# Optimization experiments

Hardware: AMD Instinct MI355X
Metric: run time of the kernel (lower is better)

The kernel has to match this reference:

```python
import jax, jax.numpy as jnp
import numpy as np

DIM = 256
HEADS = 8
HEAD_DIM = DIM // HEADS
WS = 8
EPS = 1e-5


def layernorm(x, g, b):
    mu = jnp.mean(x, axis=-1, keepdims=True)
    var = jnp.var(x, axis=-1, keepdims=True)
    return (x - mu) * jax.lax.rsqrt(var + EPS) * g + b


def partition_windows(x, ws):
    B, H, W, C = x.shape
    x = x.reshape(B, H // ws, ws, W // ws, ws, C)
    x = jnp.transpose(x, (0, 1, 3, 2, 4, 5))
    return x.reshape(B * (H // ws) * (W // ws), ws * ws, C)


def unpartition_windows(x, ws, B, H, W):
    C = x.shape[-1]
    x = x.reshape(B, H // ws, W // ws, ws, ws, C)
    x = jnp.transpose(x, (0, 1, 3, 2, 4, 5))
    return x.reshape(B, H, W, C)


def setup_inputs() -> dict:
    key = jax.random.key(0)
    ks = jax.random.split(key, 14)
    B, H, W, C = 16, 64, 64, DIM
    s_in = 1.0 / np.sqrt(C)
    s_hid = 1.0 / np.sqrt(4 * C)
    return {
        "x": jax.random.normal(ks[0], (B, H, W, C), jnp.float32),
        "ln1_g": jnp.ones((C,), jnp.float32),
        "ln1_b": jnp.zeros((C,), jnp.float32),
        "qkv_w": jax.random.uniform(ks[1], (3 * C, C), jnp.float32, -s_in, s_in),
        "qkv_b": jax.random.uniform(ks[2], (3 * C,), jnp.float32, -s_in, s_in),
        "proj_w": jax.random.uniform(ks[3], (C, C), jnp.float32, -s_in, s_in),
        "proj_b": jax.random.uniform(ks[4], (C,), jnp.float32, -s_in, s_in),
        "ln2_g": jnp.ones((C,), jnp.float32),
        "ln2_b": jnp.zeros((C,), jnp.float32),
        "ffn_w1": jax.random.uniform(ks[5], (4 * C, C), jnp.float32, -s_in, s_in),
        "ffn_b1": jax.random.uniform(ks[6], (4 * C,), jnp.float32, -s_in, s_in),
        "ffn_w2": jax.random.uniform(ks[7], (C, 4 * C), jnp.float32, -s_hid, s_hid),
        "ffn_b2": jax.random.uniform(ks[8], (C,), jnp.float32, -s_hid, s_hid),
    }


def attention(blocks, qkv_w, qkv_b, proj_w, proj_b):
    # blocks: [Bn, N, C]
    Bn, N, C = blocks.shape
    qkv = blocks @ qkv_w.T + qkv_b  # [Bn, N, 3C]
    qkv = qkv.reshape(Bn, N, 3, HEADS, HEAD_DIM)
    q, k, v = qkv[:, :, 0], qkv[:, :, 1], qkv[:, :, 2]  # each [Bn, N, h, d]
    # Faithful to the source: q @ k^T over the last two dims -> head-x-head scores per token
    scores = jnp.einsum("bnhd,bngd->bnhg", q, k) / np.sqrt(HEAD_DIM)
    attn = jax.nn.softmax(scores, axis=-1)
    out = jnp.einsum("bnhg,bngd->bnhd", attn, v).reshape(Bn, N, C)
    return out @ proj_w.T + proj_b


def reference(x, ln1_g, ln1_b, qkv_w, qkv_b, proj_w, proj_b,
              ln2_g, ln2_b, ffn_w1, ffn_b1, ffn_w2, ffn_b2):
    B, H, W, C = x.shape
    x_ = layernorm(x, ln1_g, ln1_b)
    blocks = partition_windows(x_, WS)  # [B*nW, ws*ws, C]
    out = attention(blocks, qkv_w, qkv_b, proj_w, proj_b)
    x = x + unpartition_windows(out, WS, B, H, W)
    x_ = layernorm(x, ln2_g, ln2_b)
    x_ = jax.nn.relu(x_ @ ffn_w1.T + ffn_b1) @ ffn_w2.T + ffn_b2
    return x + x_
```

## Files before the change

### kernel.cpp

```cpp
#include <hip/hip_runtime.h>
#include <hip/hip_bf16.h>
#include <stdint.h>

typedef float f32x4 __attribute__((ext_vector_type(4)));
typedef __bf16 bf16x8 __attribute__((ext_vector_type(8)));
typedef unsigned short ushort8 __attribute__((ext_vector_type(8)));

__device__ __forceinline__ float bf2f(unsigned short u) {
    unsigned int x = ((unsigned int)u) << 16;
    return __builtin_bit_cast(float, x);
}
__device__ __forceinline__ unsigned short f2bf(float f) {
    unsigned int x = __builtin_bit_cast(unsigned int, f);
    unsigned int lsb = (x >> 16) & 1u;
    x += 0x7fffu + lsb;
    return (unsigned short)(x >> 16);
}

#define GLL16(gptr, lptr)                                                      \
    __builtin_amdgcn_global_load_lds(                                          \
        (const __attribute__((address_space(1))) void*)(gptr),                 \
        (__attribute__((address_space(3))) void*)(lptr), 16, 0, 0)

__global__ __launch_bounds__(256) void cvt4_kernel(
    const float* __restrict__ w0, const float* __restrict__ w1,
    const float* __restrict__ w2, const float* __restrict__ w3,
    unsigned short* __restrict__ dst)
{
    const int i = blockIdx.x * 256 + threadIdx.x;
    const float* s; int off;
    if      (i <  49152) { s = w0; off = 0; }
    else if (i <  65536) { s = w1; off = 49152; }
    else if (i < 131072) { s = w2; off = 65536; }
    else                 { s = w3; off = 131072; }
    f32x4 v = ((const f32x4*)s)[i - off];
    ushort4 o;
    o.x = f2bf(v.x); o.y = f2bf(v.y); o.z = f2bf(v.z); o.w = f2bf(v.w);
    ((ushort4*)dst)[i] = o;
}

__global__ __launch_bounds__(256) void ln_kernel(
    const float* __restrict__ x, const float* __restrict__ g,
    const float* __restrict__ b, unsigned short* __restrict__ y)
{
    const int lane = threadIdx.x & 63, wave = threadIdx.x >> 6;
    const size_t tok = (size_t)blockIdx.x * 4 + wave;
    f32x4 v = *(const f32x4*)(x + tok * 256 + lane * 4);
    float s = v.x + v.y + v.z + v.w;
    float q = v.x * v.x + v.y * v.y + v.z * v.z + v.w * v.w;
#pragma unroll
    for (int o = 32; o; o >>= 1) {
        s += __shfl_xor(s, o, 64);
        q += __shfl_xor(q, o, 64);
    }
    float mean = s * (1.f / 256.f);
    float var  = q * (1.f / 256.f) - mean * mean;
    float rstd = rsqrtf(var + 1e-5f);
    f32x4 gr = *(const f32x4*)(g + lane * 4);
    f32x4 br = *(const f32x4*)(b + lane * 4);
    ushort4 o4;
    o4.x = f2bf((v.x - mean) * rstd * gr.x + br.x);
    o4.y = f2bf((v.y - mean) * rstd * gr.y + br.y);
    o4.z = f2bf((v.z - mean) * rstd * gr.z + br.z);
    o4.w = f2bf((v.w - mean) * rstd * gr.w + br.w);
    *(ushort4*)(y + tok * 256 + lane * 4) = o4;
}

template <int RELU, int HASRES, int OUTF32>
__global__ __launch_bounds__(256) void gemm_bt(
    const unsigned short* __restrict__ A,
    const unsigned short* __restrict__ W,
    const float* __restrict__ bias,
    const float* res,
    void* Cv,
    int M, int N, int K, int nby)
{
    __shared__ __align__(16) unsigned short As[128 * 64];
    __shared__ __align__(16) unsigned short Bs[128 * 64];

    const int t    = threadIdx.x;
    const int id   = blockIdx.x;
    const int xcd  = id & 7;
    const int sl   = id >> 3;
    const int by   = sl % nby;
    const int bx   = (sl / nby) * 8 + xcd;
    const int m0   = bx * 128;
    const int n0   = by * 128;
    const int lane = t & 63;
    const int wave = t >> 6;
    const int wm = wave & 1, wn = wave >> 1;
    const int lr = lane & 15, kc = lane >> 4;

    f32x4 acc[4][4] = {};

    const int rA   = t >> 3;
    const int gcol = ((t & 7) ^ (rA & 7)) * 8;
    const unsigned short* gA = A + (size_t)(m0 + rA) * K + gcol;
    const unsigned short* gB = W + (size_t)(n0 + rA) * K + gcol;

    for (int k0 = 0; k0 < K; k0 += 64) {
#pragma unroll
        for (int w = 0; w < 4; ++w) {
            GLL16(gA + (size_t)(w * 32) * K + k0, &As[(w * 256 + t) * 8]);
            GLL16(gB + (size_t)(w * 32) * K + k0, &Bs[(w * 256 + t) * 8]);
        }
        __syncthreads();

#pragma unroll
        for (int hh = 0; hh < 2; ++hh) {
            bf16x8 af[4], bf[4];
#pragma unroll
            for (int i = 0; i < 4; ++i) {
                const int ra = wm * 64 + i * 16 + lr;
                const int rb = wn * 64 + i * 16 + lr;
                af[i] = *(const bf16x8*)&As[ra * 64 + ((hh * 4 + kc) ^ (ra & 7)) * 8];
                bf[i] = *(const bf16x8*)&Bs[rb * 64 + ((hh * 4 + kc) ^ (rb & 7)) * 8];
            }
#pragma unroll
            for (int i = 0; i < 4; ++i)
#pragma unroll
                for (int j = 0; j < 4; ++j)
                    acc[i][j] = __builtin_amdgcn_mfma_f32_16x16x32_bf16(
                        af[i], bf[j], acc[i][j], 0, 0, 0);
        }
        __syncthreads();
    }

    float* Cf = (float*)Cv;
    unsigned short* Cb = (unsigned short*)Cv;
    const int row0 = m0 + wm * 64;
    const int col0 = n0 + wn * 64;
    const int cl = lane & 15;
    const int rq = (lane >> 4) * 4;
#pragma unroll
    for (int i = 0; i < 4; ++i) {
#pragma unroll
        for (int j = 0; j < 4; ++j) {
            const int col = col0 + j * 16 + cl;
            const float bv = bias[col];
#pragma unroll
            for (int r = 0; r < 4; ++r) {
                const int row = row0 + i * 16 + rq + r;
                float v = acc[i][j][r] + bv;
                if (RELU) v = fmaxf(v, 0.f);
                const size_t o = (size_t)row * N + col;
                if (HASRES) v += res[o];
                if (OUTF32) Cf[o] = v;
                else        Cb[o] = f2bf(v);
            }
        }
    }
}

__global__ __launch_bounds__(256) void attn_headmix(
    const unsigned short* __restrict__ qkv,
    unsigned short* __restrict__ out,
    int T)
{
    const int lane = threadIdx.x & 63, wave = threadIdx.x >> 6;
    const int tok = blockIdx.x * 4 + wave;
    if (tok >= T) return;
    const unsigned short* base = qkv + (size_t)tok * 768;
    const int h = lane >> 3, g = lane & 7;

    float s = 0.f;
#pragma unroll
    for (int d8 = 0; d8 < 4; ++d8) {
        ushort4 qa = *(const ushort4*)(base + h * 32 + d8 * 8);
        ushort4 qb = *(const ushort4*)(base + h * 32 + d8 * 8 + 4);
        ushort4 ka = *(const ushort4*)(base + 256 + g * 32 + d8 * 8);
        ushort4 kb = *(const ushort4*)(base + 256 + g * 32 + d8 * 8 + 4);
        s += bf2f(qa.x) * bf2f(ka.x) + bf2f(qa.y) * bf2f(ka.y)
           + bf2f(qa.z) * bf2f(ka.z) + bf2f(qa.w) * bf2f(ka.w)
           + bf2f(qb.x) * bf2f(kb.x) + bf2f(qb.y) * bf2f(kb.y)
           + bf2f(qb.z) * bf2f(kb.z) + bf2f(qb.w) * bf2f(kb.w);
    }
    s *= 0.17677669529663687f;

    float mx = s;
#pragma unroll
    for (int o = 1; o < 8; o <<= 1) mx = fmaxf(mx, __shfl_xor(mx, o, 64));
    float e = __expf(s - mx);
    float sum = e;
#pragma unroll
    for (int o = 1; o < 8; o <<= 1) sum += __shfl_xor(sum, o, 64);
    const float a = e / sum;

    float o0 = 0.f, o1 = 0.f, o2 = 0.f, o3 = 0.f;
#pragma unroll
    for (int gg = 0; gg < 8; ++gg) {
        const float ag = __shfl(a, (lane & 56) | gg, 64);
        ushort4 vv = *(const ushort4*)(base + 512 + gg * 32 + g * 4);
        o0 += ag * bf2f(vv.x);
        o1 += ag * bf2f(vv.y);
        o2 += ag * bf2f(vv.z);
        o3 += ag * bf2f(vv.w);
    }
    ushort4 ov;
    ov.x = f2bf(o0); ov.y = f2bf(o1); ov.z = f2bf(o2); ov.w = f2bf(o3);
    *(ushort4*)(out + (size_t)tok * 256 + lane * 4) = ov;
}

__global__ __launch_bounds__(512, 2) void ffn_fused(
    float* xo,
    const float* __restrict__ ln2_g, const float* __restrict__ ln2_b,
    const unsigned short* __restrict__ w1,
    const float* __restrict__ b1p,
    const unsigned short* __restrict__ w2,
    const float* __restrict__ b2p)
{
    __shared__ __align__(16) unsigned short U[32768];
    __shared__ __align__(16) unsigned short W1a[16384];
    __shared__ __align__(16) unsigned short W2a[16384];
    __shared__ __align__(16) unsigned short Hs[2][8192];

    unsigned short* const W1b = U;
    unsigned short* const W2b = U + 16384;

    const int t = threadIdx.x;
    const int lane = t & 63, wave = t >> 6;
    const int m0 = blockIdx.x * 128;
    const int lr = lane & 15, kc = lane >> 4;
    const int cl = lane & 15, rq = (lane >> 4) * 4;
    const int wm = wave & 1, wn = wave >> 1;

    const int r1b = t >> 5;
    const int sc1 = t & 31;
    const int gc1 = (sc1 & ~7) | ((sc1 & 7) ^ (r1b & 7));
    const int r2b = t >> 3;
    const int gc2 = (t & 7) ^ (r2b & 7);

    #define STAGE_W1(hp, W1t)                                                  \
        do {                                                                   \
            _Pragma("unroll")                                                  \
            for (int j = 0; j < 4; ++j)                                        \
                GLL16(w1 + (size_t)((hp) * 64 + j * 16 + r1b) * 256 + gc1 * 8, \
                      &(W1t)[(j * 512 + t) * 8]);                              \
        } while (0)
    #define STAGE_W2(hp, W2t)                                                  \
        do {                                                                   \
            _Pragma("unroll")                                                  \
            for (int j = 0; j < 4; ++j)                                        \
                GLL16(w2 + (size_t)(j * 64 + r2b) * 1024 + (hp) * 64 + gc2 * 8,\
                      &(W2t)[(j * 512 + t) * 8]);                              \
        } while (0)

    STAGE_W1(0, W1a);
    STAGE_W2(0, W2a);

    {
        const int row0 = t >> 2;
        const int seg  = t & 3;
        const float* xrp = xo + (size_t)(m0 + row0) * 256 + seg * 64;
        f32x4 xv[16];
#pragma unroll
        for (int i = 0; i < 16; ++i) xv[i] = ((const f32x4*)xrp)[i];
        float s = 0.f, q = 0.f;
#pragma unroll
        for (int i = 0; i < 16; ++i) {
            s += xv[i].x + xv[i].y + xv[i].z + xv[i].w;
            q += xv[i].x * xv[i].x + xv[i].y * xv[i].y
               + xv[i].z * xv[i].z + xv[i].w * xv[i].w;
        }
        s += __shfl_xor(s, 1, 64); q += __shfl_xor(q, 1, 64);
        s += __shfl_xor(s, 2, 64); q += __shfl_xor(q, 2, 64);
        const float mean = s * (1.f / 256.f);
        const float rstd = rsqrtf(q * (1.f / 256.f) - mean * mean + 1e-5f);
#pragma unroll
        for (int c8 = 0; c8 < 8; ++c8) {
            const f32x4 g0 = ((const f32x4*)(ln2_g + seg * 64 + c8 * 8))[0];
            const f32x4 g1 = ((const f32x4*)(ln2_g + seg * 64 + c8 * 8))[1];
            const f32x4 bb0 = ((const f32x4*)(ln2_b + seg * 64 + c8 * 8))[0];
            const f32x4 bb1 = ((const f32x4*)(ln2_b + seg * 64 + c8 * 8))[1];
            const f32x4 a0 = xv[c8 * 2], a1 = xv[c8 * 2 + 1];
            ushort8 o;
            o[0] = f2bf((a0.x - mean) * rstd * g0.x + bb0.x);
            o[1] = f2bf((a0.y - mean) * rstd * g0.y + bb0.y);
            o[2] = f2bf((a0.z - mean) * rstd * g0.z + bb0.z);
            o[3] = f2bf((a0.w - mean) * rstd * g0.w + bb0.w);
            o[4] = f2bf((a1.x - mean) * rstd * g1.x + bb1.x);
            o[5] = f2bf((a1.y - mean) * rstd * g1.y + bb1.y);
            o[6] = f2bf((a1.z - mean) * rstd * g1.z + bb1.z);
            o[7] = f2bf((a1.w - mean) * rstd * g1.w + bb1.w);
            const int gc = seg * 8 + c8;
            const int sc = (gc & ~7) | ((gc & 7) ^ (row0 & 7));
            *(ushort8*)&U[row0 * 256 + sc * 8] = o;
        }
    }
    __syncthreads();

    bf16x8 afr[4][8];
#pragma unroll
    for (int i = 0; i < 4; ++i) {
        const int ra = wm * 64 + i * 16 + lr;
#pragma unroll
        for (int ks = 0; ks < 8; ++ks) {
            const int c = ks * 4 + kc;
            afr[i][ks] = *(const bf16x8*)
                &U[ra * 256 + ((c & ~7) | ((c & 7) ^ (ra & 7))) * 8];
        }
    }
    __syncthreads();
    STAGE_W1(1, W1b);

    f32x4 acc[4][4] = {};

    #define HPHASE(hcv, W1c, Hbuf)                                             \
        do {                                                                   \
            f32x4 acch[4] = {};                                                \
            __builtin_amdgcn_s_setprio(1);                                     \
            _Pragma("unroll")                                                  \
            for (int ks = 0; ks < 8; ++ks) {                                   \
                const int c = ks * 4 + kc;                                     \
                const int rb = wn * 16 + lr;                                   \
                const bf16x8 bfr = *(const bf16x8*)                            \
                    &(W1c)[rb * 256 + ((c & ~7) | ((c & 7) ^ (rb & 7))) * 8];  \
                _Pragma("unroll")                                              \
                for (int i = 0; i < 4; ++i)                                    \
                    acch[i] = __builtin_amdgcn_mfma_f32_16x16x32_bf16(         \
                        bfr, afr[i][ks], acch[i], 0, 0, 0);                    \
            }                                                                  \
            __builtin_amdgcn_s_setprio(0);                                     \
            const f32x4 bv = *(const f32x4*)(b1p + (hcv) * 64 + wn * 16 + rq); \
            const int sbase = wn * 2 + (rq >> 3);                              \
            _Pragma("unroll")                                                  \
            for (int i = 0; i < 4; ++i) {                                      \
                const int tok = wm * 64 + i * 16 + cl;                         \
                ushort4 o;                                                     \
                o.x = f2bf(fmaxf(acch[i][0] + bv.x, 0.f));                     \
                o.y = f2bf(fmaxf(acch[i][1] + bv.y, 0.f));                     \
                o.z = f2bf(fmaxf(acch[i][2] + bv.z, 0.f));                     \
                o.w = f2bf(fmaxf(acch[i][3] + bv.w, 0.f));                     \
                *(ushort4*)&(Hbuf)[tok * 64 + ((sbase ^ (tok & 7)) * 8)        \
                                   + (rq & 4)] = o;                            \
            }                                                                  \
        } while (0)

    #define OPHASE(W2c, Hbuf)                                                  \
        do {                                                                   \
            _Pragma("unroll")                                                  \
            for (int ks = 0; ks < 2; ++ks) {                                   \
                const int c = ks * 4 + kc;                                     \
                bf16x8 bw[4];                                                  \
                _Pragma("unroll")                                              \
                for (int j = 0; j < 4; ++j) {                                  \
                    const int rb = wn * 64 + j * 16 + lr;                      \
                    bw[j] = *(const bf16x8*)                                   \
                        &(W2c)[rb * 64 + ((c ^ (rb & 7)) * 8)];                \
                }                                                              \
                __builtin_amdgcn_s_setprio(1);                                 \
                _Pragma("unroll")                                              \
                for (int i = 0; i < 4; ++i) {                                  \
                    const int ra = wm * 64 + i * 16 + lr;                      \
                    const bf16x8 ah = *(const bf16x8*)                         \
                        &(Hbuf)[ra * 64 + ((c ^ (ra & 7)) * 8)];               \
                    _Pragma("unroll")                                          \
                    for (int j = 0; j < 4; ++j)                                \
                        acc[i][j] = __builtin_amdgcn_mfma_f32_16x16x32_bf16(   \
                            ah, bw[j], acc[i][j], 0, 0, 0);                    \
                }                                                              \
                __builtin_amdgcn_s_setprio(0);                                 \
            }                                                                  \
        } while (0)

    HPHASE(0, W1a, Hs[0]);
    __syncthreads();

    for (int hc = 0; hc < 16; ++hc) {
        if (hc < 14) STAGE_W1(hc + 2, (hc & 1) ? W1b : W1a);
        if (hc < 15) STAGE_W2(hc + 1, (hc & 1) ? W2a : W2b);
        if (hc < 15) HPHASE(hc + 1, (hc & 1) ? W1a : W1b, Hs[(hc + 1) & 1]);
        OPHASE((hc & 1) ? W2b : W2a, Hs[hc & 1]);
        __syncthreads();
    }

    const int rqe = (lane >> 4) * 4;
#pragma unroll
    for (int i = 0; i < 4; ++i)
#pragma unroll
        for (int j = 0; j < 4; ++j) {
            const int col = wn * 64 + j * 16 + cl;
            const float bv = b2p[col];
#pragma unroll
            for (int r = 0; r < 4; ++r) {
                const int row = m0 + wm * 64 + i * 16 + rqe + r;
                const size_t o = (size_t)row * 256 + col;
                xo[o] = acc[i][j][r] + bv + xo[o];
            }
        }
    #undef STAGE_W1
    #undef STAGE_W2
    #undef HPHASE
    #undef OPHASE
}

extern "C" void kernel_launch(void* const* d_in, const int* in_sizes, int n_in,
                              void* d_out, int out_size, void* d_ws, size_t ws_size,
                              hipStream_t stream)
{
    const float* x      = (const float*)d_in[0];
    const float* ln1_g  = (const float*)d_in[1];
    const float* ln1_b  = (const float*)d_in[2];
    const float* qkv_w  = (const float*)d_in[3];
    const float* qkv_b  = (const float*)d_in[4];
    const float* proj_w = (const float*)d_in[5];
    const float* proj_b = (const float*)d_in[6];
    const float* ln2_g  = (const float*)d_in[7];
    const float* ln2_b  = (const float*)d_in[8];
    const float* ffn_w1 = (const float*)d_in[9];
    const float* ffn_b1 = (const float*)d_in[10];
    const float* ffn_w2 = (const float*)d_in[11];
    const float* ffn_b2 = (const float*)d_in[12];
    float* xo = (float*)d_out;

    const int M = 65536;
    const size_t MEG = 1024 * 1024;
    unsigned short* ws = (unsigned short*)d_ws;
    unsigned short* qkv_wb  = ws;
    unsigned short* proj_wb = ws + 196608;
    unsigned short* ffn_w1b = ws + 262144;
    unsigned short* ffn_w2b = ws + 524288;
    unsigned short* xn   = ws + 1 * MEG;
    unsigned short* att  = ws + 17 * MEG;
    unsigned short* qkvb = ws + 33 * MEG;

    cvt4_kernel<<<768, 256, 0, stream>>>(qkv_w, proj_w, ffn_w1, ffn_w2, ws);

    ln_kernel<<<M / 4, 256, 0, stream>>>(x, ln1_g, ln1_b, xn);
    gemm_bt<0, 0, 0><<<3072, 256, 0, stream>>>(
        xn, qkv_wb, qkv_b, nullptr, qkvb, M, 768, 256, 6);
    attn_headmix<<<M / 4, 256, 0, stream>>>(qkvb, att, M);
    gemm_bt<0, 1, 1><<<1024, 256, 0, stream>>>(
        att, proj_wb, proj_b, x, xo, M, 256, 256, 2);
    ffn_fused<<<M / 128, 512, 0, stream>>>(
        xo, ln2_g, ln2_b, ffn_w1b, ffn_b1, ffn_w2b, ffn_b2);
}
```

Baseline: 413.7 us.

## Use partial vmcnt waits and non-draining barriers in fused FFN pipeline

Replaces the __syncthreads in the FFN hidden-chunk loop with explicit s_waitcnt vmcnt(N) plus an LDS-only wait and raw s_barrier. Async global-to-LDS weight loads for the next stage can then stay in flight across barriers instead of being drained each iteration. The loop is peeled into prologue and epilogue so the wait counts stay exact, and the b1 bias loads are prefetched one chunk ahead. The cost is fragile hand-counted vmcnt values: a miscount would read stale or incomplete LDS tiles.

```diff
diff --git a/kernel.cpp b/kernel.cpp
--- a/kernel.cpp
+++ b/kernel.cpp
@@ -21,6 +21,14 @@
     __builtin_amdgcn_global_load_lds(                                          \
         (const __attribute__((address_space(1))) void*)(gptr),                 \
         (__attribute__((address_space(3))) void*)(lptr), 16, 0, 0)
+
+#define VMWAIT(N)                                                              \
+    do { asm volatile("s_waitcnt vmcnt(" #N ")" ::: "memory"); } while (0)
+#define BARRIER_NODRAIN()                                                      \
+    do {                                                                       \
+        asm volatile("s_waitcnt lgkmcnt(0)" ::: "memory");                     \
+        __builtin_amdgcn_s_barrier();                                          \
+    } while (0)
 
 __global__ __launch_bounds__(256) void cvt4_kernel(
     const float* __restrict__ w0, const float* __restrict__ w1,
@@ -247,6 +255,7 @@
 
     STAGE_W1(0, W1a);
     STAGE_W2(0, W2a);
+    f32x4 bvc = *(const f32x4*)(b1p + wn * 16 + rq);
 
     {
         const int row0 = t >> 2;
@@ -301,11 +310,10 @@
         }
     }
     __syncthreads();
-    STAGE_W1(1, W1b);
 
     f32x4 acc[4][4] = {};
 
-    #define HPHASE(hcv, W1c, Hbuf)                                             \
+    #define HPHASE(bv, W1c, Hbuf)                                              \
         do {                                                                   \
             f32x4 acch[4] = {};                                                \
             __builtin_amdgcn_s_setprio(1);                                     \
@@ -321,16 +329,15 @@
                         bfr, afr[i][ks], acch[i], 0, 0, 0);                    \
             }                                                                  \
             __builtin_amdgcn_s_setprio(0);                                     \
-            const f32x4 bv = *(const f32x4*)(b1p + (hcv) * 64 + wn * 16 + rq); \
             const int sbase = wn * 2 + (rq >> 3);                              \
             _Pragma("unroll")                                                  \
             for (int i = 0; i < 4; ++i) {                                      \
                 const int tok = wm * 64 + i * 16 + cl;                         \
                 ushort4 o;                                                     \
-                o.x = f2bf(fmaxf(acch[i][0] + bv.x, 0.f));                     \
-                o.y = f2bf(fmaxf(acch[i][1] + bv.y, 0.f));                     \
-                o.z = f2bf(fmaxf(acch[i][2] + bv.z, 0.f));                     \
-                o.w = f2bf(fmaxf(acch[i][3] + bv.w, 0.f));                     \
+                o.x = f2bf(fmaxf(acch[i][0] + (bv).x, 0.f));                   \
+                o.y = f2bf(fmaxf(acch[i][1] + (bv).y, 0.f));                   \
+                o.z = f2bf(fmaxf(acch[i][2] + (bv).z, 0.f));                   \
+                o.w = f2bf(fmaxf(acch[i][3] + (bv).w, 0.f));                   \
                 *(ushort4*)&(Hbuf)[tok * 64 + ((sbase ^ (tok & 7)) * 8)        \
                                    + (rq & 4)] = o;                            \
             }                                                                  \
@@ -363,16 +370,44 @@
             }                                                                  \
         } while (0)
 
-    HPHASE(0, W1a, Hs[0]);
-    __syncthreads();
-
-    for (int hc = 0; hc < 16; ++hc) {
-        if (hc < 14) STAGE_W1(hc + 2, (hc & 1) ? W1b : W1a);
-        if (hc < 15) STAGE_W2(hc + 1, (hc & 1) ? W2a : W2b);
-        if (hc < 15) HPHASE(hc + 1, (hc & 1) ? W1a : W1b, Hs[(hc + 1) & 1]);
-        OPHASE((hc & 1) ? W2b : W2a, Hs[hc & 1]);
-        __syncthreads();
-    }
+    STAGE_W1(1, W1b);
+    f32x4 bvn = *(const f32x4*)(b1p + 1 * 64 + wn * 16 + rq);
+    HPHASE(bvc, W1a, Hs[0]);
+    BARRIER_NODRAIN();
+    bvc = bvn;
+
+    STAGE_W1(2, W1a);
+    STAGE_W2(1, W2b);
+    bvn = *(const f32x4*)(b1p + 2 * 64 + wn * 16 + rq);
+    VMWAIT(9);
+    HPHASE(bvc, W1b, Hs[1]);
+    OPHASE(W2a, Hs[0]);
+    BARRIER_NODRAIN();
+    bvc = bvn;
+
+    for (int hc = 1; hc <= 13; ++hc) {
+        unsigned short* const w1dst = (hc & 1) ? W1b : W1a;
+        unsigned short* const w2dst = (hc & 1) ? W2a : W2b;
+        unsigned short* const w1src = (hc & 1) ? W1a : W1b;
+        unsigned short* const w2src = (hc & 1) ? W2b : W2a;
+        STAGE_W1(hc + 2, w1dst);
+        STAGE_W2(hc + 1, w2dst);
+        bvn = *(const f32x4*)(b1p + (hc + 2) * 64 + wn * 16 + rq);
+        VMWAIT(9);
+        HPHASE(bvc, w1src, Hs[(hc + 1) & 1]);
+        OPHASE(w2src, Hs[hc & 1]);
+        BARRIER_NODRAIN();
+        bvc = bvn;
+    }
+
+    STAGE_W2(15, W2b);
+    VMWAIT(4);
+    HPHASE(bvc, W1b, Hs[1]);
+    OPHASE(W2a, Hs[0]);
+    BARRIER_NODRAIN();
+
+    VMWAIT(0);
+    OPHASE(W2b, Hs[1]);
 
     const int rqe = (lane >> 4) * 4;
 #pragma unroll
```

Measured after the change: 406.9 us. No clear change (-1.6%).

## Fuse head-mixing attention into the projection GEMM via shared memory

Applied to the files above, without the earlier changes.

Merges the per-token head-mix attention kernel with the output projection GEMM. Each 512-thread block computes attention for 128 tokens, writes the bf16 result into a swizzled LDS tile, then runs MFMA against double-buffered projection weights and adds bias and residual. This drops the 32 MB round trip of the attention intermediate through global memory and one kernel launch. The cost is 128 KB of LDS per block and a serial attention phase before the GEMM, which may limit occupancy and overlap.

```diff
diff --git a/kernel.cpp b/kernel.cpp
--- a/kernel.cpp
+++ b/kernel.cpp
@@ -152,53 +152,135 @@
     }
 }
 
-__global__ __launch_bounds__(256) void attn_headmix(
+__global__ __launch_bounds__(512, 2) void proj_attn(
     const unsigned short* __restrict__ qkv,
-    unsigned short* __restrict__ out,
-    int T)
+    const unsigned short* __restrict__ wp,
+    const float* __restrict__ bias,
+    const float* __restrict__ res,
+    float* __restrict__ out)
 {
-    const int lane = threadIdx.x & 63, wave = threadIdx.x >> 6;
-    const int tok = blockIdx.x * 4 + wave;
-    if (tok >= T) return;
-    const unsigned short* base = qkv + (size_t)tok * 768;
+    __shared__ __align__(16) unsigned short U[128 * 256];
+    __shared__ __align__(16) unsigned short Wk[2][16384];
+
+    const int t = threadIdx.x;
+    const int lane = t & 63, wave = t >> 6;
+    const int m0 = blockIdx.x * 128;
+    const int lr = lane & 15, kc = lane >> 4;
+    const int cl = lane & 15, rq = (lane >> 4) * 4;
+    const int wm = wave & 1, wn = wave >> 1;
+
+    const int r2b = t >> 3;
+    const int gc2 = (t & 7) ^ (r2b & 7);
+
+    #define STAGE_WP(kc4, Wt)                                                  \
+        do {                                                                   \
+            _Pragma("unroll")                                                  \
+            for (int j = 0; j < 4; ++j)                                        \
+                GLL16(wp + (size_t)(j * 64 + r2b) * 256 + (kc4) * 64 + gc2 * 8,\
+                      &(Wt)[(j * 512 + t) * 8]);                               \
+        } while (0)
+
+    STAGE_WP(0, Wk[0]);
+    STAGE_WP(1, Wk[1]);
+
     const int h = lane >> 3, g = lane & 7;
-
-    float s = 0.f;
-#pragma unroll
-    for (int d8 = 0; d8 < 4; ++d8) {
-        ushort4 qa = *(const ushort4*)(base + h * 32 + d8 * 8);
-        ushort4 qb = *(const ushort4*)(base + h * 32 + d8 * 8 + 4);
-        ushort4 ka = *(const ushort4*)(base + 256 + g * 32 + d8 * 8);
-        ushort4 kb = *(const ushort4*)(base + 256 + g * 32 + d8 * 8 + 4);
-        s += bf2f(qa.x) * bf2f(ka.x) + bf2f(qa.y) * bf2f(ka.y)
-           + bf2f(qa.z) * bf2f(ka.z) + bf2f(qa.w) * bf2f(ka.w)
-           + bf2f(qb.x) * bf2f(kb.x) + bf2f(qb.y) * bf2f(kb.y)
-           + bf2f(qb.z) * bf2f(kb.z) + bf2f(qb.w) * bf2f(kb.w);
-    }
-    s *= 0.17677669529663687f;
-
-    float mx = s;
-#pragma unroll
-    for (int o = 1; o < 8; o <<= 1) mx = fmaxf(mx, __shfl_xor(mx, o, 64));
-    float e = __expf(s - mx);
-    float sum = e;
-#pragma unroll
-    for (int o = 1; o < 8; o <<= 1) sum += __shfl_xor(sum, o, 64);
-    const float a = e / sum;
-
-    float o0 = 0.f, o1 = 0.f, o2 = 0.f, o3 = 0.f;
-#pragma unroll
-    for (int gg = 0; gg < 8; ++gg) {
-        const float ag = __shfl(a, (lane & 56) | gg, 64);
-        ushort4 vv = *(const ushort4*)(base + 512 + gg * 32 + g * 4);
-        o0 += ag * bf2f(vv.x);
-        o1 += ag * bf2f(vv.y);
-        o2 += ag * bf2f(vv.z);
-        o3 += ag * bf2f(vv.w);
-    }
-    ushort4 ov;
-    ov.x = f2bf(o0); ov.y = f2bf(o1); ov.z = f2bf(o2); ov.w = f2bf(o3);
-    *(ushort4*)(out + (size_t)tok * 256 + lane * 4) = ov;
+    for (int p = 0; p < 16; ++p) {
+        const int row = p * 8 + wave;
+        const unsigned short* base = qkv + (size_t)(m0 + row) * 768;
+
+        float s = 0.f;
+#pragma unroll
+        for (int d8 = 0; d8 < 4; ++d8) {
+            ushort4 qa = *(const ushort4*)(base + h * 32 + d8 * 8);
+            ushort4 qb = *(const ushort4*)(base + h * 32 + d8 * 8 + 4);
+            ushort4 ka = *(const ushort4*)(base + 256 + g * 32 + d8 * 8);
+            ushort4 kb = *(const ushort4*)(base + 256 + g * 32 + d8 * 8 + 4);
+            s += bf2f(qa.x) * bf2f(ka.x) + bf2f(qa.y) * bf2f(ka.y)
+               + bf2f(qa.z) * bf2f(ka.z) + bf2f(qa.w) * bf2f(ka.w)
+               + bf2f(qb.x) * bf2f(kb.x) + bf2f(qb.y) * bf2f(kb.y)
+               + bf2f(qb.z) * bf2f(kb.z) + bf2f(qb.w) * bf2f(kb.w);
+        }
+        s *= 0.17677669529663687f;
+
+        float mx = s;
+#pragma unroll
+        for (int o = 1; o < 8; o <<= 1) mx = fmaxf(mx, __shfl_xor(mx, o, 64));
+        float e = __expf(s - mx);
+        float sum = e;
+#pragma unroll
+        for (int o = 1; o < 8; o <<= 1) sum += __shfl_xor(sum, o, 64);
+        const float a = e / sum;
+
+        float o0 = 0.f, o1 = 0.f, o2 = 0.f, o3 = 0.f;
+#pragma unroll
+        for (int gg = 0; gg < 8; ++gg) {
+            const float ag = __shfl(a, (lane & 56) | gg, 64);
+            ushort4 vv = *(const ushort4*)(base + 512 + gg * 32 + g * 4);
+            o0 += ag * bf2f(vv.x);
+            o1 += ag * bf2f(vv.y);
+            o2 += ag * bf2f(vv.z);
+            o3 += ag * bf2f(vv.w);
+        }
+        const int gcu = lane >> 1;
+        const int sc = (gcu & ~7) | ((gcu & 7) ^ (row & 7));
+        ushort4 ov;
+        ov.x = f2bf(o0); ov.y = f2bf(o1); ov.z = f2bf(o2); ov.w = f2bf(o3);
+        *(ushort4*)&U[row * 256 + sc * 8 + (lane & 1) * 4] = ov;
+    }
+    __syncthreads();
+
+    bf16x8 afr[4][8];
+#pragma unroll
+    for (int i = 0; i < 4; ++i) {
+        const int ra = wm * 64 + i * 16 + lr;
+#pragma unroll
+        for (int ks = 0; ks < 8; ++ks) {
+            const int c = ks * 4 + kc;
+            afr[i][ks] = *(const bf16x8*)
+                &U[ra * 256 + ((c & ~7) | ((c & 7) ^ (ra & 7))) * 8];
+        }
+    }
+
+    f32x4 acc[4][4] = {};
+    for (int c4 = 0; c4 < 4; ++c4) {
+        if (c4 >= 2) __syncthreads();
+        const unsigned short* Wc = Wk[c4 & 1];
+#pragma unroll
+        for (int kk = 0; kk < 2; ++kk) {
+            const int c = kk * 4 + kc;
+            bf16x8 bw[4];
+#pragma unroll
+            for (int j = 0; j < 4; ++j) {
+                const int rb = wn * 64 + j * 16 + lr;
+                bw[j] = *(const bf16x8*)&Wc[rb * 64 + ((c ^ (rb & 7)) * 8)];
+            }
+#pragma unroll
+            for (int i = 0; i < 4; ++i)
+#pragma unroll
+                for (int j = 0; j < 4; ++j)
+                    acc[i][j] = __builtin_amdgcn_mfma_f32_16x16x32_bf16(
+                        afr[i][c4 * 2 + kk], bw[j], acc[i][j], 0, 0, 0);
+        }
+        if (c4 < 2) {
+            __syncthreads();
+            STAGE_WP(c4 + 2, Wk[c4 & 1]);
+        }
+    }
+
+#pragma unroll
+    for (int i = 0; i < 4; ++i)
+#pragma unroll
+        for (int j = 0; j < 4; ++j) {
+            const int col = wn * 64 + j * 16 + cl;
+            const float bv = bias[col];
+#pragma unroll
+            for (int r = 0; r < 4; ++r) {
+                const int row = m0 + wm * 64 + i * 16 + rq + r;
+                const size_t o = (size_t)row * 256 + col;
+                out[o] = acc[i][j][r] + bv + res[o];
+            }
+        }
+    #undef STAGE_WP
 }
 
 __global__ __launch_bounds__(512, 2) void ffn_fused(
@@ -421,7 +503,6 @@
     unsigned short* ffn_w1b = ws + 262144;
     unsigned short* ffn_w2b = ws + 524288;
     unsigned short* xn   = ws + 1 * MEG;
-    unsigned short* att  = ws + 17 * MEG;
     unsigned short* qkvb = ws + 33 * MEG;
 
     cvt4_kernel<<<768, 256, 0, stream>>>(qkv_w, proj_w, ffn_w1, ffn_w2, ws);
@@ -429,9 +510,8 @@
     ln_kernel<<<M / 4, 256, 0, stream>>>(x, ln1_g, ln1_b, xn);
     gemm_bt<0, 0, 0><<<3072, 256, 0, stream>>>(
         xn, qkv_wb, qkv_b, nullptr, qkvb, M, 768, 256, 6);
-    attn_headmix<<<M / 4, 256, 0, stream>>>(qkvb, att, M);
-    gemm_bt<0, 1, 1><<<1024, 256, 0, stream>>>(
-        att, proj_wb, proj_b, x, xo, M, 256, 256, 2);
+    proj_attn<<<M / 128, 512, 0, stream>>>(
+        qkvb, proj_wb, proj_b, x, xo);
     ffn_fused<<<M / 128, 512, 0, stream>>>(
         xo, ln2_g, ln2_b, ffn_w1b, ffn_b1, ffn_w2b, ffn_b2);
 }
```

New measurement: 343.6 us. -17.0%, faster.
